# Kernel optimization log

Measured on AMD Instinct MI355X. Metric: run time of the kernel, lower is better.

## Reference

```python
import jax, jax.numpy as jnp
import numpy as np

B, S, E, H = 4, 2048, 1024, 16
D = E // H  # head dim = 64
NEG = -1e9


def setup_inputs() -> dict:
    key = jax.random.key(0)
    ks = jax.random.split(key, 6)
    scale = 1.0 / np.sqrt(E)
    return {
        "x": jax.random.normal(ks[0], (B, S, E), dtype=jnp.float32),
        "in_proj_weight": jax.random.normal(ks[1], (3 * E, E), dtype=jnp.float32) * scale,
        "in_proj_bias": jax.random.normal(ks[2], (3 * E,), dtype=jnp.float32) * 0.02,
        "out_proj_weight": jax.random.normal(ks[3], (E, E), dtype=jnp.float32) * scale,
        "out_proj_bias": jax.random.normal(ks[4], (E,), dtype=jnp.float32) * 0.02,
        "mask": jax.random.randint(ks[5], (B, S), 0, 2, dtype=jnp.int32),
    }


def reference(x, in_proj_weight, in_proj_bias, out_proj_weight, out_proj_bias, mask):
    # Equivalent of F.multi_head_attention_forward(h,h,h,...) with batch-first x.
    # qkv projection: [B,S,3E]
    qkv = jnp.einsum("bse,fe->bsf", x, in_proj_weight) + in_proj_bias
    q, k, v = jnp.split(qkv, 3, axis=-1)
    # split heads -> [B,S,H,D]
    q = q.reshape(B, S, H, D) * (1.0 / np.sqrt(D))
    k = k.reshape(B, S, H, D)
    v = v.reshape(B, S, H, D)
    # scores [B,H,Sq,Sk]
    scores = jnp.einsum("bqhd,bkhd->bhqk", q, k)
    # key_padding_mask = (mask == 0): True positions are excluded
    pad = (mask == 0)[:, None, None, :]  # [B,1,1,Sk]
    scores = jnp.where(pad, NEG, scores)
    attn = jax.nn.softmax(scores, axis=-1)
    # attention output -> [B,S,E]
    ctx = jnp.einsum("bhqk,bkhd->bqhd", attn, v).reshape(B, S, E)
    h_ = jnp.einsum("bse,fe->bsf", ctx, out_proj_weight) + out_proj_bias
    # residual; dropout is identity in eval mode
    return x + h_
```

## Files before the change

### kernel.cpp

```cpp
#include <hip/hip_runtime.h>
#include <stdint.h>
#include <math.h>

#define B_ 4
#define S_ 2048
#define E_ 1024
#define H_ 16
#define D_ 64
#define M_ (B_*S_)

typedef __attribute__((ext_vector_type(8))) short bf16x8;
typedef __attribute__((ext_vector_type(4))) float f32x4;

__device__ __forceinline__ unsigned short f2bf(float f) {
  union { float f; uint32_t u; } v; v.f = f;
  uint32_t u = v.u;
  return (unsigned short)((u + 0x7FFFu + ((u >> 16) & 1u)) >> 16);
}

__device__ __forceinline__ void gload16(const void* g, void* l) {
  __builtin_amdgcn_global_load_lds(
      (__attribute__((address_space(1))) void*)g,
      (__attribute__((address_space(3))) void*)l, 16, 0, 0);
}

__device__ __forceinline__ uint32_t cvtpk(float lo, float hi) {
  uint32_t r;
  asm("v_cvt_pk_bf16_f32 %0, %1, %2" : "=v"(r) : "v"(lo), "v"(hi));
  return r;
}

#define N1 ((M_*E_)/4)
#define N2 ((3*E_*E_)/4)
#define N3 ((E_*E_)/4)
#define NM ((B_*S_)/4)
__global__ __launch_bounds__(256) void cvt_all(const float* __restrict__ x,
                                               const float* __restrict__ w1,
                                               const float* __restrict__ w2,
                                               const int* __restrict__ mask,
                                               unsigned short* __restrict__ dst,
                                               float* __restrict__ maskf) {
  int i = blockIdx.x * 256 + threadIdx.x;
  if (i < N1 + N2 + N3) {
    const float* src;
    int j;
    if (i < N1) { src = x; j = i; }
    else if (i < N1 + N2) { src = w1; j = i - N1; }
    else { src = w2; j = i - N1 - N2; }
    float4 v = reinterpret_cast<const float4*>(src)[j];
    ushort4 o;
    o.x = f2bf(v.x); o.y = f2bf(v.y); o.z = f2bf(v.z); o.w = f2bf(v.w);
    reinterpret_cast<ushort4*>(dst)[i] = o;
  } else if (i < N1 + N2 + N3 + NM) {
    int j = i - (N1 + N2 + N3);
    int4 m = reinterpret_cast<const int4*>(mask)[j];
    float4 o;
    o.x = m.x ? 0.0f : -2.0e9f;
    o.y = m.y ? 0.0f : -2.0e9f;
    o.z = m.z ? 0.0f : -2.0e9f;
    o.w = m.w ? 0.0f : -2.0e9f;
    reinterpret_cast<float4*>(maskf)[j] = o;
  }
}

__global__ __launch_bounds__(256) void gemm_qkv128(
    const unsigned short* __restrict__ A,
    const unsigned short* __restrict__ W,
    const float* __restrict__ bias,
    unsigned short* __restrict__ Qg,
    unsigned short* __restrict__ Kg,
    unsigned short* __restrict__ Vtg)
{
  __shared__ __align__(16) unsigned short SMEM[128*136];
  unsigned short* As = SMEM;
  unsigned short* Bs = SMEM + 4096;
  const int tid = threadIdx.x;
  const int lane = tid & 63;
  const int wave = tid >> 6;
  const int wm = (wave >> 1) * 64, wn = (wave & 1) * 64;
  const int l15 = lane & 15, lg = lane >> 4;

  const int orig = blockIdx.y * 24 + blockIdx.x;
  const int xcd = orig & 7;
  const int idx = orig >> 3;
  const int tn = (xcd * 3 + (idx % 3)) * 128;
  const int tm = (idx / 3) * 128;

  f32x4 zero4 = {0.f, 0.f, 0.f, 0.f};
  f32x4 acc[4][4];
  #pragma unroll
  for (int mi = 0; mi < 4; ++mi)
    #pragma unroll
    for (int ni = 0; ni < 4; ++ni) acc[mi][ni] = zero4;

  const int r0 = tid >> 2, c0 = (tid & 3) * 8;
  const unsigned short* Arow0 = A + (size_t)(tm + r0) * E_ + c0;
  const unsigned short* Arow1 = A + (size_t)(tm + r0 + 64) * E_ + c0;
  const unsigned short* Wrow0 = W + (size_t)(tn + r0) * E_ + c0;
  const unsigned short* Wrow1 = W + (size_t)(tn + r0 + 64) * E_ + c0;
  unsigned short* lA0 = As + tid * 8;
  unsigned short* lA1 = As + (tid + 256) * 8;
  unsigned short* lB0 = Bs + tid * 8;
  unsigned short* lB1 = Bs + (tid + 256) * 8;

  for (int k0 = 0; k0 < E_; k0 += 32) {
    gload16(Arow0 + k0, lA0);
    gload16(Arow1 + k0, lA1);
    gload16(Wrow0 + k0, lB0);
    gload16(Wrow1 + k0, lB1);
    __syncthreads();
    bf16x8 af[4], bfm[4];
    #pragma unroll
    for (int mi = 0; mi < 4; ++mi)
      af[mi] = *(const bf16x8*)&As[(wm + mi*16 + l15)*32 + lg*8];
    #pragma unroll
    for (int ni = 0; ni < 4; ++ni)
      bfm[ni] = *(const bf16x8*)&Bs[(wn + ni*16 + l15)*32 + lg*8];
    #pragma unroll
    for (int mi = 0; mi < 4; ++mi)
      #pragma unroll
      for (int ni = 0; ni < 4; ++ni)
        acc[mi][ni] = __builtin_amdgcn_mfma_f32_16x16x32_bf16(af[mi], bfm[ni], acc[mi][ni], 0, 0, 0);
    __syncthreads();
  }

  const int sec = tn >> 10;
  if (sec < 2) {
    #pragma unroll
    for (int ni = 0; ni < 4; ++ni) {
      const int col = tn + wn + ni*16 + l15;
      const float bcol = bias[col];
      const int f2 = col & 1023;
      const int h = f2 >> 6, d = f2 & 63;
      #pragma unroll
      for (int mi = 0; mi < 4; ++mi) {
        #pragma unroll
        for (int r = 0; r < 4; ++r) {
          const int row = tm + wm + mi*16 + lg*4 + r;
          const int b = row >> 11, s = row & (S_-1);
          const size_t bh = (size_t)(b * H_ + h);
          float val = acc[mi][ni][r] + bcol;
          if (sec == 0) {
            Qg[(bh*S_ + s)*D_ + d] = f2bf(val * 0.18033688f);
          } else {
            const int ch = (d >> 3) ^ (s & 7);
            Kg[(bh*S_ + s)*D_ + ch*8 + (d & 7)] = f2bf(val);
          }
        }
      }
    }
  } else {
    __syncthreads();
    unsigned short* T = SMEM;
    #pragma unroll
    for (int ni = 0; ni < 4; ++ni) {
      const int f = wn + ni*16 + l15;
      const float bcol = bias[tn + f];
      #pragma unroll
      for (int mi = 0; mi < 4; ++mi) {
        const int s0 = wm + mi*16 + lg*4;
        uint2 p;
        p.x = cvtpk(acc[mi][ni][0] + bcol, acc[mi][ni][1] + bcol);
        p.y = cvtpk(acc[mi][ni][2] + bcol, acc[mi][ni][3] + bcol);
        *reinterpret_cast<uint2*>(&T[f*136 + s0]) = p;
      }
    }
    __syncthreads();
    const int f = tid >> 1, sch = tid & 1;
    const int d = f & 63, hl = f >> 6;
    const int h = ((tn & 1023) >> 6) + hl;
    const int b = tm >> 11;
    const size_t bh = (size_t)(b * H_ + h);
    const int sbase = (tm & (S_-1)) + sch*64;
    unsigned short* vout = Vtg + (bh*D_ + d)*S_ + sbase;
    const unsigned short* tin = &T[f*136 + sch*64];
    #pragma unroll
    for (int j = 0; j < 8; ++j) {
      uint4 v = *reinterpret_cast<const uint4*>(&tin[j*8]);
      *reinterpret_cast<uint4*>(&vout[(j ^ (d & 7))*8]) = v;
    }
  }
}

__global__ __launch_bounds__(512, 4) void attn_fwd(
    const unsigned short* __restrict__ Qg,
    const unsigned short* __restrict__ Kg,
    const unsigned short* __restrict__ Vtg,
    const float* __restrict__ maskf,
    unsigned short* __restrict__ ctx)
{
  __shared__ __align__(16) unsigned char SMEM[36864];
  unsigned short* KsP = (unsigned short*)SMEM;
  unsigned short* VsP = (unsigned short*)(SMEM + 16384);
  const int tid = threadIdx.x, lane = tid & 63, wave = tid >> 6;
  const int l15 = lane & 15, lg = lane >> 4;

  const int lin = blockIdx.x;
  const int bh = (lin & 7) * 8 + (lin >> 6);
  const int qi = (lin >> 3) & 7;
  const int b = bh >> 4, h = bh & 15;
  const int q0 = qi * 256 + wave * 32;

  const unsigned short* Qb = Qg + (size_t)bh * S_ * D_;
  const unsigned short* Kb = Kg + (size_t)bh * S_ * D_;
  const unsigned short* Vb = Vtg + (size_t)bh * D_ * S_;
  const float* mrow = maskf + b * S_;

  bf16x8 qf[2][2];
  #pragma unroll
  for (int mi = 0; mi < 2; ++mi)
    #pragma unroll
    for (int kc = 0; kc < 2; ++kc)
      qf[mi][kc] = *(const bf16x8*)&Qb[(size_t)(q0 + mi*16 + l15)*D_ + kc*32 + lg*8];

  f32x4 zero4 = {0.f, 0.f, 0.f, 0.f};
  f32x4 accO[2][4];
  f32x4 accL[2] = {zero4, zero4};
  #pragma unroll
  for (int mi = 0; mi < 2; ++mi)
    #pragma unroll
    for (int df = 0; df < 4; ++df) accO[mi][df] = zero4;

  union { uint32_t u[4]; bf16x8 v; } ou;
  ou.u[0] = ou.u[1] = ou.u[2] = ou.u[3] = 0x3F803F80u;
  const bf16x8 onesv = ou.v;

  int kboff0[4], kboff1[4], vboff0[4], vboff1[4];
  #pragma unroll
  for (int kt = 0; kt < 4; ++kt) {
    const int krow = kt*16 + l15;
    kboff0[kt] = (krow*64 + ((lg ^ (krow & 7))*8)) * 2;
    kboff1[kt] = (krow*64 + (((4+lg) ^ (krow & 7))*8)) * 2;
  }
  #pragma unroll
  for (int df = 0; df < 4; ++df) {
    const int vrow = df*16 + l15;
    vboff0[df] = (vrow*64 + ((lg ^ (vrow & 7))*8)) * 2;
    vboff1[df] = (vrow*64 + (((4+lg) ^ (vrow & 7))*8)) * 2;
  }
  const char* KsB = (const char*)KsP;
  const char* VsB = (const char*)VsP;

  const int sr0 = tid >> 3, sc0 = (tid & 7) * 8;

  gload16(Kb + (size_t)sr0 * D_ + sc0, KsP + tid*8);
  gload16(Vb + (size_t)sr0 * S_ + sc0, VsP + tid*8);
  f32x4 mv0[4], mv1[4];
  #pragma unroll
  for (int kt = 0; kt < 4; ++kt)
    mv0[kt] = *(const f32x4*)&mrow[kt*16 + lg*4];
  const unsigned short* kpre = Kb + (size_t)(64 + sr0) * D_ + sc0;
  const unsigned short* vpre = Vb + (size_t)sr0 * S_ + 64 + sc0;
  const float* mpre = mrow + 64 + lg*4;
  __syncthreads();

#define ATTN_TILE(CUR, MVC, MVN, DO_PF)                                         \
  {                                                                             \
    if (DO_PF) {                                                                \
      gload16(kpre, KsP + ((CUR)^1)*4096 + tid*8);                              \
      gload16(vpre, VsP + ((CUR)^1)*4096 + tid*8);                              \
      kpre += 64*D_; vpre += 64;                                                \
      _Pragma("unroll")                                                         \
      for (int kt = 0; kt < 4; ++kt)                                            \
        MVN[kt] = *(const f32x4*)&mpre[kt*16];                                  \
      mpre += 64;                                                               \
    }                                                                           \
    f32x4 s_[2][4];                                                             \
    __builtin_amdgcn_s_setprio(1);                                              \
    _Pragma("unroll")                                                           \
    for (int kt = 0; kt < 4; ++kt) {                                            \
      bf16x8 kf0 = *(const bf16x8*)(KsB + (CUR)*8192 + kboff0[kt]);             \
      bf16x8 kf1 = *(const bf16x8*)(KsB + (CUR)*8192 + kboff1[kt]);             \
      s_[0][kt] = __builtin_amdgcn_mfma_f32_16x16x32_bf16(kf0, qf[0][0], MVC[kt], 0, 0, 0); \
      s_[0][kt] = __builtin_amdgcn_mfma_f32_16x16x32_bf16(kf1, qf[0][1], s_[0][kt], 0, 0, 0); \
      s_[1][kt] = __builtin_amdgcn_mfma_f32_16x16x32_bf16(kf0, qf[1][0], MVC[kt], 0, 0, 0); \
      s_[1][kt] = __builtin_amdgcn_mfma_f32_16x16x32_bf16(kf1, qf[1][1], s_[1][kt], 0, 0, 0); \
    }                                                                           \
    __builtin_amdgcn_s_setprio(0);                                              \
    _Pragma("unroll")                                                           \
    for (int mi = 0; mi < 2; ++mi)                                              \
      _Pragma("unroll")                                                         \
      for (int kt = 0; kt < 4; ++kt)                                            \
        _Pragma("unroll")                                                       \
        for (int r = 0; r < 4; ++r)                                             \
          s_[mi][kt][r] = __builtin_amdgcn_exp2f(s_[mi][kt][r]);                \
    bf16x8 pa[2][2];                                                            \
    _Pragma("unroll")                                                           \
    for (int mi = 0; mi < 2; ++mi) {                                            \
      _Pragma("unroll")                                                         \
      for (int kk = 0; kk < 2; ++kk) {                                          \
        uint32_t a0 = cvtpk(s_[mi][2*kk][0],   s_[mi][2*kk][1]);                \
        uint32_t c1 = cvtpk(s_[mi][2*kk][2],   s_[mi][2*kk][3]);                \
        uint32_t b0 = cvtpk(s_[mi][2*kk+1][0], s_[mi][2*kk+1][1]);              \
        uint32_t d1 = cvtpk(s_[mi][2*kk+1][2], s_[mi][2*kk+1][3]);              \
        asm("v_permlane32_swap_b32 %0, %1" : "+v"(a0), "+v"(b0));               \
        asm("v_permlane16_swap_b32 %0, %1" : "+v"(a0), "+v"(b0));               \
        asm("v_permlane32_swap_b32 %0, %1" : "+v"(c1), "+v"(d1));               \
        asm("v_permlane16_swap_b32 %0, %1" : "+v"(c1), "+v"(d1));               \
        union { bf16x8 v; uint32_t u[4]; } w;                                   \
        w.u[0] = a0; w.u[1] = c1; w.u[2] = b0; w.u[3] = d1;                     \
        pa[mi][kk] = w.v;                                                       \
      }                                                                         \
    }                                                                           \
    __builtin_amdgcn_s_setprio(1);                                              \
    accL[0] = __builtin_amdgcn_mfma_f32_16x16x32_bf16(pa[0][0], onesv, accL[0], 0, 0, 0); \
    accL[1] = __builtin_amdgcn_mfma_f32_16x16x32_bf16(pa[1][0], onesv, accL[1], 0, 0, 0); \
    _Pragma("unroll")                                                           \
    for (int df = 0; df < 4; ++df) {                                            \
      bf16x8 vf = *(const bf16x8*)(VsB + (CUR)*8192 + vboff0[df]);              \
      accO[0][df] = __builtin_amdgcn_mfma_f32_16x16x32_bf16(pa[0][0], vf, accO[0][df], 0, 0, 0); \
      accO[1][df] = __builtin_amdgcn_mfma_f32_16x16x32_bf16(pa[1][0], vf, accO[1][df], 0, 0, 0); \
    }                                                                           \
    accL[0] = __builtin_amdgcn_mfma_f32_16x16x32_bf16(pa[0][1], onesv, accL[0], 0, 0, 0); \
    accL[1] = __builtin_amdgcn_mfma_f32_16x16x32_bf16(pa[1][1], onesv, accL[1], 0, 0, 0); \
    _Pragma("unroll")                                                           \
    for (int df = 0; df < 4; ++df) {                                            \
      bf16x8 vf = *(const bf16x8*)(VsB + (CUR)*8192 + vboff1[df]);              \
      accO[0][df] = __builtin_amdgcn_mfma_f32_16x16x32_bf16(pa[0][1], vf, accO[0][df], 0, 0, 0); \
      accO[1][df] = __builtin_amdgcn_mfma_f32_16x16x32_bf16(pa[1][1], vf, accO[1][df], 0, 0, 0); \
    }                                                                           \
    __builtin_amdgcn_s_setprio(0);                                              \
    __syncthreads();                                                            \
  }

  for (int tt = 0; tt < 32; tt += 2) {
    ATTN_TILE(0, mv0, mv1, 1)
    ATTN_TILE(1, mv1, mv0, (tt < 30))
  }
#undef ATTN_TILE

  unsigned short* T = (unsigned short*)SMEM + wave * 2304;
  #pragma unroll
  for (int mi = 0; mi < 2; ++mi) {
    #pragma unroll
    for (int r = 0; r < 4; ++r) {
      const float iv = 1.0f / accL[mi][r];
      const int q = mi*16 + lg*4 + r;
      #pragma unroll
      for (int df = 0; df < 4; ++df)
        T[q*72 + df*16 + l15] = f2bf(accO[mi][df][r] * iv);
    }
  }
  __syncthreads();
  {
    const int g = lane >> 2, c4 = lane & 3;
    #pragma unroll
    for (int j = 0; j < 4; ++j) {
      const int t = j*16 + g;
      const int q = t >> 1, half = t & 1;
      uint4 v = *reinterpret_cast<const uint4*>(&T[q*72 + half*32 + c4*8]);
      const int srow = q0 + q;
      *reinterpret_cast<uint4*>(&ctx[((size_t)b*S_ + srow)*E_ + h*D_ + half*32 + c4*8]) = v;
    }
  }
}

__global__ __launch_bounds__(256) void gemm_out(
    const unsigned short* __restrict__ A,
    const unsigned short* __restrict__ W,
    const float* __restrict__ bias,
    const float* __restrict__ xres,
    float* __restrict__ out)
{
  __shared__ __align__(16) unsigned short As[128*32];
  __shared__ __align__(16) unsigned short Bs[128*32];
  const int tid = threadIdx.x;
  const int lane = tid & 63;
  const int wave = tid >> 6;
  const int wm = (wave >> 1) * 64, wn = (wave & 1) * 64;
  const int tm = blockIdx.y * 128, tn = blockIdx.x * 128;
  const int l15 = lane & 15, lg = lane >> 4;

  f32x4 zero4 = {0.f, 0.f, 0.f, 0.f};
  f32x4 acc[4][4];
  #pragma unroll
  for (int mi = 0; mi < 4; ++mi)
    #pragma unroll
    for (int ni = 0; ni < 4; ++ni) acc[mi][ni] = zero4;

  const int r0 = tid >> 2, c0 = (tid & 3) * 8;
  const unsigned short* Arow0 = A + (size_t)(tm + r0) * E_ + c0;
  const unsigned short* Arow1 = A + (size_t)(tm + r0 + 64) * E_ + c0;
  const unsigned short* Wrow0 = W + (size_t)(tn + r0) * E_ + c0;
  const unsigned short* Wrow1 = W + (size_t)(tn + r0 + 64) * E_ + c0;
  unsigned short* lA0 = As + tid * 8;
  unsigned short* lA1 = As + (tid + 256) * 8;
  unsigned short* lB0 = Bs + tid * 8;
  unsigned short* lB1 = Bs + (tid + 256) * 8;

  for (int k0 = 0; k0 < E_; k0 += 32) {
    gload16(Arow0 + k0, lA0);
    gload16(Arow1 + k0, lA1);
    gload16(Wrow0 + k0, lB0);
    gload16(Wrow1 + k0, lB1);
    __syncthreads();
    bf16x8 af[4], bfm[4];
    #pragma unroll
    for (int mi = 0; mi < 4; ++mi)
      af[mi] = *(const bf16x8*)&As[(wm + mi*16 + l15)*32 + lg*8];
    #pragma unroll
    for (int ni = 0; ni < 4; ++ni)
      bfm[ni] = *(const bf16x8*)&Bs[(wn + ni*16 + l15)*32 + lg*8];
    #pragma unroll
    for (int mi = 0; mi < 4; ++mi)
      #pragma unroll
      for (int ni = 0; ni < 4; ++ni)
        acc[mi][ni] = __builtin_amdgcn_mfma_f32_16x16x32_bf16(af[mi], bfm[ni], acc[mi][ni], 0, 0, 0);
    __syncthreads();
  }

  #pragma unroll
  for (int ni = 0; ni < 4; ++ni) {
    const int col = tn + wn + ni*16 + l15;
    const float bcol = bias[col];
    #pragma unroll
    for (int mi = 0; mi < 4; ++mi) {
      #pragma unroll
      for (int r = 0; r < 4; ++r) {
        const int row = tm + wm + mi*16 + lg*4 + r;
        out[(size_t)row*E_ + col] = xres[(size_t)row*E_ + col] + acc[mi][ni][r] + bcol;
      }
    }
  }
}

extern "C" void kernel_launch(void* const* d_in, const int* in_sizes, int n_in,
                              void* d_out, int out_size, void* d_ws, size_t ws_size,
                              hipStream_t stream) {
  const float* x  = (const float*)d_in[0];
  const float* w1 = (const float*)d_in[1];
  const float* b1 = (const float*)d_in[2];
  const float* w2 = (const float*)d_in[3];
  const float* b2 = (const float*)d_in[4];
  const int* mask = (const int*)d_in[5];
  float* out = (float*)d_out;

  const size_t SZ = (size_t)B_*H_*S_*D_;
  unsigned short* Qg  = (unsigned short*)d_ws;
  unsigned short* Kg  = Qg + SZ;
  unsigned short* Vtg = Kg + SZ;
  unsigned short* xb  = Vtg + SZ;
  unsigned short* w1b = xb + (size_t)M_*E_;
  unsigned short* w2b = w1b + (size_t)3*E_*E_;
  float* maskf = (float*)(w2b + (size_t)E_*E_);
  unsigned short* ctx = xb;

  const int ntot = N1 + N2 + N3 + NM;
  cvt_all<<<(ntot + 255)/256, 256, 0, stream>>>(x, w1, w2, mask, xb, maskf);

  gemm_qkv128<<<dim3(24, 64), 256, 0, stream>>>(xb, w1b, b1, Qg, Kg, Vtg);
  attn_fwd<<<512, 512, 0, stream>>>(Qg, Kg, Vtg, maskf, ctx);
  gemm_out<<<dim3(E_/128, M_/128), 256, 0, stream>>>(ctx, w2b, b2, x, out);
}
```

Baseline: 210.2 us.

## Deepen QKV GEMM K-step with swizzled LDS and halve attention block size

The QKV GEMM now loads 64-wide K slices per iteration into an XOR-swizzled LDS layout. This halves the number of barrier pairs and is meant to avoid bank conflicts on the fragment reads. The attention kernel drops from 512-thread blocks (256 queries) to 256-thread blocks (128 queries), twice as many blocks. Each thread now issues two K/V tile loads per stage, and the XCD-aware block mapping is reworked, aiming for better occupancy and load balance. The tradeoffs are that each K/V tile is reused by fewer query rows, and the LDS footprint for the GEMM doubles.

```diff
diff --git a/kernel.cpp b/kernel.cpp
--- a/kernel.cpp
+++ b/kernel.cpp
@@ -71,9 +71,9 @@
     unsigned short* __restrict__ Kg,
     unsigned short* __restrict__ Vtg)
 {
-  __shared__ __align__(16) unsigned short SMEM[128*136];
+  __shared__ __align__(16) unsigned short SMEM[17408];
   unsigned short* As = SMEM;
-  unsigned short* Bs = SMEM + 4096;
+  unsigned short* Bs = SMEM + 8192;
   const int tid = threadIdx.x;
   const int lane = tid & 63;
   const int wave = tid >> 6;
@@ -93,34 +93,44 @@
     #pragma unroll
     for (int ni = 0; ni < 4; ++ni) acc[mi][ni] = zero4;
 
-  const int r0 = tid >> 2, c0 = (tid & 3) * 8;
-  const unsigned short* Arow0 = A + (size_t)(tm + r0) * E_ + c0;
-  const unsigned short* Arow1 = A + (size_t)(tm + r0 + 64) * E_ + c0;
-  const unsigned short* Wrow0 = W + (size_t)(tn + r0) * E_ + c0;
-  const unsigned short* Wrow1 = W + (size_t)(tn + r0 + 64) * E_ + c0;
-  unsigned short* lA0 = As + tid * 8;
-  unsigned short* lA1 = As + (tid + 256) * 8;
-  unsigned short* lB0 = Bs + tid * 8;
-  unsigned short* lB1 = Bs + (tid + 256) * 8;
-
-  for (int k0 = 0; k0 < E_; k0 += 32) {
-    gload16(Arow0 + k0, lA0);
-    gload16(Arow1 + k0, lA1);
-    gload16(Wrow0 + k0, lB0);
-    gload16(Wrow1 + k0, lB1);
-    __syncthreads();
-    bf16x8 af[4], bfm[4];
-    #pragma unroll
-    for (int mi = 0; mi < 4; ++mi)
-      af[mi] = *(const bf16x8*)&As[(wm + mi*16 + l15)*32 + lg*8];
-    #pragma unroll
-    for (int ni = 0; ni < 4; ++ni)
-      bfm[ni] = *(const bf16x8*)&Bs[(wn + ni*16 + l15)*32 + lg*8];
-    #pragma unroll
-    for (int mi = 0; mi < 4; ++mi)
+  const int r0 = tid >> 3;
+  const int cg = ((tid & 7) ^ (r0 & 7)) * 8;
+  const unsigned short* Abase = A + (size_t)(tm + r0) * E_ + cg;
+  const unsigned short* Bbase = W + (size_t)(tn + r0) * E_ + cg;
+  unsigned short* lA = As + tid * 8;
+  unsigned short* lB = Bs + tid * 8;
+
+  int aoff[4], boff[4];
+  #pragma unroll
+  for (int i = 0; i < 4; ++i) {
+    aoff[i] = (wm + i*16 + l15)*64 + ((lg ^ (l15 & 7)) * 8);
+    boff[i] = (wn + i*16 + l15)*64 + ((lg ^ (l15 & 7)) * 8);
+  }
+  const int x4a = ((lg ^ 4 ^ (l15 & 7)) * 8) - ((lg ^ (l15 & 7)) * 8);
+
+  for (int k0 = 0; k0 < E_; k0 += 64) {
+    #pragma unroll
+    for (int j = 0; j < 4; ++j)
+      gload16(Abase + k0 + j*32*E_, lA + j*2048);
+    #pragma unroll
+    for (int j = 0; j < 4; ++j)
+      gload16(Bbase + k0 + j*32*E_, lB + j*2048);
+    __syncthreads();
+    #pragma unroll
+    for (int kc = 0; kc < 2; ++kc) {
+      bf16x8 af[4], bfv[4];
+      #pragma unroll
+      for (int mi = 0; mi < 4; ++mi)
+        af[mi] = *(const bf16x8*)&As[aoff[mi] + kc*x4a];
       #pragma unroll
       for (int ni = 0; ni < 4; ++ni)
-        acc[mi][ni] = __builtin_amdgcn_mfma_f32_16x16x32_bf16(af[mi], bfm[ni], acc[mi][ni], 0, 0, 0);
+        bfv[ni] = *(const bf16x8*)&Bs[boff[ni] + kc*x4a];
+      #pragma unroll
+      for (int mi = 0; mi < 4; ++mi)
+        #pragma unroll
+        for (int ni = 0; ni < 4; ++ni)
+          acc[mi][ni] = __builtin_amdgcn_mfma_f32_16x16x32_bf16(af[mi], bfv[ni], acc[mi][ni], 0, 0, 0);
+    }
     __syncthreads();
   }
 
@@ -182,24 +192,26 @@
   }
 }
 
-__global__ __launch_bounds__(512, 4) void attn_fwd(
+__global__ __launch_bounds__(256, 5) void attn_fwd(
     const unsigned short* __restrict__ Qg,
     const unsigned short* __restrict__ Kg,
     const unsigned short* __restrict__ Vtg,
     const float* __restrict__ maskf,
     unsigned short* __restrict__ ctx)
 {
-  __shared__ __align__(16) unsigned char SMEM[36864];
+  __shared__ __align__(16) unsigned char SMEM[32768];
   unsigned short* KsP = (unsigned short*)SMEM;
   unsigned short* VsP = (unsigned short*)(SMEM + 16384);
   const int tid = threadIdx.x, lane = tid & 63, wave = tid >> 6;
   const int l15 = lane & 15, lg = lane >> 4;
 
   const int lin = blockIdx.x;
-  const int bh = (lin & 7) * 8 + (lin >> 6);
-  const int qi = (lin >> 3) & 7;
+  const int xcd = lin & 7;
+  const int j = lin >> 3;
+  const int bh = xcd * 8 + (j & 7);
+  const int qi = j >> 3;
   const int b = bh >> 4, h = bh & 15;
-  const int q0 = qi * 256 + wave * 32;
+  const int q0 = qi * 128 + wave * 32;
 
   const unsigned short* Qb = Qg + (size_t)bh * S_ * D_;
   const unsigned short* Kb = Kg + (size_t)bh * S_ * D_;
@@ -244,7 +256,9 @@
   const int sr0 = tid >> 3, sc0 = (tid & 7) * 8;
 
   gload16(Kb + (size_t)sr0 * D_ + sc0, KsP + tid*8);
+  gload16(Kb + (size_t)(sr0 + 32) * D_ + sc0, KsP + (tid+256)*8);
   gload16(Vb + (size_t)sr0 * S_ + sc0, VsP + tid*8);
+  gload16(Vb + (size_t)(sr0 + 32) * S_ + sc0, VsP + (tid+256)*8);
   f32x4 mv0[4], mv1[4];
   #pragma unroll
   for (int kt = 0; kt < 4; ++kt)
@@ -258,7 +272,9 @@
   {                                                                             \
     if (DO_PF) {                                                                \
       gload16(kpre, KsP + ((CUR)^1)*4096 + tid*8);                              \
+      gload16(kpre + 32*D_, KsP + ((CUR)^1)*4096 + (tid+256)*8);                \
       gload16(vpre, VsP + ((CUR)^1)*4096 + tid*8);                              \
+      gload16(vpre + 32*S_, VsP + ((CUR)^1)*4096 + (tid+256)*8);                \
       kpre += 64*D_; vpre += 64;                                                \
       _Pragma("unroll")                                                         \
       for (int kt = 0; kt < 4; ++kt)                                            \
@@ -345,8 +361,8 @@
   {
     const int g = lane >> 2, c4 = lane & 3;
     #pragma unroll
-    for (int j = 0; j < 4; ++j) {
-      const int t = j*16 + g;
+    for (int j2 = 0; j2 < 4; ++j2) {
+      const int t = j2*16 + g;
       const int q = t >> 1, half = t & 1;
       uint4 v = *reinterpret_cast<const uint4*>(&T[q*72 + half*32 + c4*8]);
       const int srow = q0 + q;
@@ -449,6 +465,6 @@
   cvt_all<<<(ntot + 255)/256, 256, 0, stream>>>(x, w1, w2, mask, xb, maskf);
 
   gemm_qkv128<<<dim3(24, 64), 256, 0, stream>>>(xb, w1b, b1, Qg, Kg, Vtg);
-  attn_fwd<<<512, 512, 0, stream>>>(Qg, Kg, Vtg, maskf, ctx);
+  attn_fwd<<<1024, 256, 0, stream>>>(Qg, Kg, Vtg, maskf, ctx);
   gemm_out<<<dim3(E_/128, M_/128), 256, 0, stream>>>(ctx, w2b, b2, x, out);
 }
```

Result: slower. 514.7 us (+144.9%).
